# Kernel tuning notes

Measured on AMD Instinct MI355X. Metric: run time of the kernel, lower is better.

## Reference

```python
import jax, jax.numpy as jnp
import numpy as np

NUM_HEADS = 8

def setup_inputs() -> dict:
    key = jax.random.key(0)
    ks = jax.random.split(key, 12)
    B, C, H, W = 4, 256, 64, 64
    QK = 256
    NSP = 256
    x = jax.random.normal(ks[0], (B, C, H, W), dtype=jnp.float32)
    affinity_matrix = jax.random.uniform(ks[1], (B, NSP, H * W), dtype=jnp.float32)
    norm_w = 1.0 + 0.02 * jax.random.normal(ks[2], (C,), dtype=jnp.float32)
    norm_b = 0.02 * jax.random.normal(ks[3], (C,), dtype=jnp.float32)
    Wq = 0.02 * jax.random.normal(ks[4], (QK, C), dtype=jnp.float32)
    Wk = 0.02 * jax.random.normal(ks[5], (QK, C), dtype=jnp.float32)
    Wv = 0.02 * jax.random.normal(ks[6], (C, C), dtype=jnp.float32)
    Wsp = 0.02 * jax.random.normal(ks[7], (QK, C), dtype=jnp.float32)
    lepe_w = 0.02 * jax.random.normal(ks[8], (C, 1, 3, 3), dtype=jnp.float32)  # depthwise OIHW
    lepe_b = 0.02 * jax.random.normal(ks[9], (C,), dtype=jnp.float32)
    return {"x": x, "affinity_matrix": affinity_matrix, "norm_w": norm_w,
            "norm_b": norm_b, "Wq": Wq, "Wk": Wk, "Wv": Wv, "Wsp": Wsp,
            "lepe_w": lepe_w, "lepe_b": lepe_b, "num_spixels": NSP}


def _layernorm2d(x, w, b, eps=1e-6):
    # LayerNorm over channel dim of NCHW input
    xp = x.transpose(0, 2, 3, 1)  # B,H,W,C
    mu = xp.mean(-1, keepdims=True)
    var = ((xp - mu) ** 2).mean(-1, keepdims=True)
    xn = (xp - mu) * jax.lax.rsqrt(var + eps) * w + b
    return xn.transpose(0, 3, 1, 2)


def _sgca(x, affinity_matrix, norm_w, norm_b, Wq, Wk, Wv, Wsp, lepe_w, lepe_b, num_spixels):
    B, C, H, W = x.shape
    HW = H * W
    h = NUM_HEADS
    qk_dim = Wq.shape[0]
    dqk = qk_dim // h
    dv = C // h
    scale = (C // h) ** -0.5

    xn = _layernorm2d(x, norm_w, norm_b)

    # superpixel aggregation: b (hw) c
    x_flat = xn.reshape(B, C, HW).transpose(0, 2, 1)  # B,HW,C
    stoken = jnp.einsum('bmn,bnc->bmc', affinity_matrix, x_flat)
    stoken = stoken / (affinity_matrix.sum(-1, keepdims=True) + 1e-16)  # B,nsp,C

    # sp projection -> B,h,dqk,nsp
    st = jnp.einsum('bmc,qc->bmq', stoken, Wsp).transpose(0, 2, 1)
    st = st.reshape(B, h, dqk, num_spixels)

    # 1x1 conv projections
    q = jnp.einsum('oc,bchw->bohw', Wq, xn).reshape(B, h, dqk, HW)
    k = jnp.einsum('oc,bchw->bohw', Wk, xn).reshape(B, h, dqk, HW)
    vx = jnp.einsum('oc,bchw->bohw', Wv, xn)  # B,C,H,W
    v = vx.reshape(B, h, dv, HW)

    # LePE: depthwise 3x3 conv on v(x)
    lepe = jax.lax.conv_general_dilated(
        vx, lepe_w, window_strides=(1, 1), padding=((1, 1), (1, 1)),
        feature_group_count=C, dimension_numbers=('NCHW', 'OIHW', 'NCHW'))
    lepe = lepe + lepe_b[None, :, None, None]
    # faithful to original: [B,C,HW] -> permute -> [B,HW,C] -> reshape B,C,H,W
    lepe = lepe.reshape(B, C, HW).transpose(0, 2, 1).reshape(B, C, H, W)

    # stage 1: k^T @ stoken, softmax over HW axis
    s_attn = jnp.einsum('bhdn,bhdm->bhnm', k, st) * scale  # B,h,HW,nsp
    s_attn = jax.nn.softmax(s_attn, axis=-2)
    s_out = jnp.einsum('bhdn,bhnm->bhdm', v, s_attn)  # B,h,dv,nsp

    # stage 2: stoken^T @ q, softmax over nsp axis
    x_attn = jnp.einsum('bhdm,bhdn->bhmn', st, q) * scale  # B,h,nsp,HW
    x_attn = jax.nn.softmax(x_attn, axis=-2)
    x_out = jnp.einsum('bhdm,bhmn->bhdn', s_out, x_attn).reshape(B, C, H, W)

    return x_out + lepe


def reference(x, affinity_matrix, norm_w, norm_b, Wq, Wk, Wv, Wsp, lepe_w, lepe_b, num_spixels):
    return _sgca(x, affinity_matrix, norm_w, norm_b, Wq, Wk, Wv, Wsp, lepe_w, lepe_b, num_spixels)
```

## Files before the change

### kernel.cpp

```cpp
#include <hip/hip_runtime.h>
#include <hip/hip_bf16.h>

#define BATCH 4
#define CCH   256
#define HWHW  4096
#define NSP   256
#define NHEAD 8
#define SCALE 0.17677669529663689f
#define PLANE 1048576L

typedef short bf16x8 __attribute__((ext_vector_type(8)));
typedef short bf16x4 __attribute__((ext_vector_type(4)));
typedef float f32x4  __attribute__((ext_vector_type(4)));

__device__ __forceinline__ short f2bs(float f) {
    __hip_bfloat16 h = __float2bfloat16(f);
    return *(short*)&h;
}
__device__ __forceinline__ bf16x8 cvt8(float4 a, float4 b) {
    bf16x8 p;
    p[0] = f2bs(a.x); p[1] = f2bs(a.y); p[2] = f2bs(a.z); p[3] = f2bs(a.w);
    p[4] = f2bs(b.x); p[5] = f2bs(b.y); p[6] = f2bs(b.z); p[7] = f2bs(b.w);
    return p;
}
__device__ __forceinline__ void gll16(const __hip_bfloat16* g, __hip_bfloat16* l) {
    __builtin_amdgcn_global_load_lds(
        (const __attribute__((address_space(1))) unsigned int*)(const void*)g,
        (__attribute__((address_space(3))) unsigned int*)(void*)l,
        16, 0, 0);
}

__global__ __launch_bounds__(512)
void ln_fused_kernel(const float* __restrict__ x, const float* __restrict__ w,
                     const float* __restrict__ bb,
                     const float* __restrict__ Wq, const float* __restrict__ Wk,
                     const float* __restrict__ Wv, const float* __restrict__ Wsp,
                     __hip_bfloat16* __restrict__ xn_cn,
                     __hip_bfloat16* __restrict__ xn_nc,
                     __hip_bfloat16* __restrict__ wbf)
{
    __shared__ float ps[32][64], pss[32][64];
    __shared__ float mus[64], rstds[64];
    __shared__ float wls[256], bls[256];
    int blk = blockIdx.x;
    int t = threadIdx.x;
    if (blk >= 256) {
        int sel = blk - 256;
        const float* src = (sel == 0) ? Wq : (sel == 1) ? Wk : (sel == 2) ? Wv : Wsp;
        __hip_bfloat16* dst = wbf + sel * 65536;
        for (int i = t * 4; i < 65536; i += 2048) {
            float4 f = *(const float4*)(src + i);
            __hip_bfloat16 p[4];
            p[0] = __float2bfloat16(f.x); p[1] = __float2bfloat16(f.y);
            p[2] = __float2bfloat16(f.z); p[3] = __float2bfloat16(f.w);
            *(int2*)(dst + i) = *(int2*)p;
        }
        return;
    }
    int b = blk >> 6;
    int n0 = (blk & 63) * 64;
    int pg = t & 15;
    int cq = t >> 4;
    if (t < 256) { wls[t] = w[t]; bls[t] = bb[t]; }

    const float* xp = x + ((long)(b * CCH + cq * 8)) * HWHW + n0 + pg * 4;
    float4 v[8];
#pragma unroll
    for (int i = 0; i < 8; ++i) v[i] = *(const float4*)(xp + (long)i * HWHW);
    float4 s = {0.f,0.f,0.f,0.f}, ss = {0.f,0.f,0.f,0.f};
#pragma unroll
    for (int i = 0; i < 8; ++i) {
        s.x += v[i].x; s.y += v[i].y; s.z += v[i].z; s.w += v[i].w;
        ss.x += v[i].x * v[i].x; ss.y += v[i].y * v[i].y;
        ss.z += v[i].z * v[i].z; ss.w += v[i].w * v[i].w;
    }
    *(float4*)&ps[cq][pg * 4]  = s;
    *(float4*)&pss[cq][pg * 4] = ss;
    __syncthreads();
    if (t < 64) {
        float S = 0.f, SS = 0.f;
#pragma unroll
        for (int q = 0; q < 32; ++q) { S += ps[q][t]; SS += pss[q][t]; }
        float mu = S * (1.f / 256.f);
        float var = SS * (1.f / 256.f) - mu * mu;
        mus[t] = mu; rstds[t] = rsqrtf(var + 1e-6f);
    }
    __syncthreads();
    float4 mu4 = *(float4*)&mus[pg * 4];
    float4 rs4 = *(float4*)&rstds[pg * 4];

    bf16x8 pk[4];
#pragma unroll
    for (int i = 0; i < 8; ++i) {
        int c = cq * 8 + i;
        float wc = wls[c], bc = bls[c];
        short h0 = f2bs((v[i].x - mu4.x) * rs4.x * wc + bc);
        short h1 = f2bs((v[i].y - mu4.y) * rs4.y * wc + bc);
        short h2 = f2bs((v[i].z - mu4.z) * rs4.z * wc + bc);
        short h3 = f2bs((v[i].w - mu4.w) * rs4.w * wc + bc);
        pk[0][i] = h0; pk[1][i] = h1; pk[2][i] = h2; pk[3][i] = h3;
        bf16x4 q; q[0] = h0; q[1] = h1; q[2] = h2; q[3] = h3;
        *(bf16x4*)(xn_cn + ((long)(b * CCH + c)) * HWHW + n0 + pg * 4) = q;
    }
#pragma unroll
    for (int j = 0; j < 4; ++j)
        *(bf16x8*)(xn_nc + ((long)b * HWHW + n0 + pg * 4 + j) * CCH + cq * 8) = pk[j];
}

__device__ __forceinline__ void gemm_k256_oneshot(
    const __hip_bfloat16* __restrict__ A, const __hip_bfloat16* __restrict__ B,
    __hip_bfloat16* __restrict__ C, int bx, int by, int bz,
    int N, long aStrideZ, long bStrideZ, long cStrideZ,
    __hip_bfloat16* __restrict__ Asm)
{
    const int K = 256;
    const int t = threadIdx.x, lane = t & 63, w = t >> 6;
    const int l15 = lane & 15, quad = lane >> 4;
    const int Mt = by * 64, Nt = bx * 64;
    const __hip_bfloat16* aSrc = A + (long)bz * aStrideZ
        + (long)(Mt + w * 16 + l15) * K + quad * 8;
#pragma unroll
    for (int p = 0; p < 8; ++p)
        gll16(aSrc + p * 32, Asm + ((w * 8 + p) << 9));

    const int wm = (w & 1) * 2, wn = (w >> 1) * 2;
    const __hip_bfloat16* b0p = B + (long)bz * bStrideZ
        + (long)(Nt + wn * 16 + l15) * K + quad * 8;
    const __hip_bfloat16* b1p = b0p + 16 * K;
    f32x4 acc00 = {0.f,0.f,0.f,0.f}, acc01 = acc00, acc10 = acc00, acc11 = acc00;
    __syncthreads();
#pragma unroll
    for (int s = 0; s < 8; ++s) {
        bf16x8 a0 = *(const bf16x8*)&Asm[((wm * 8 + s) << 9) + lane * 8];
        bf16x8 a1 = *(const bf16x8*)&Asm[(((wm + 1) * 8 + s) << 9) + lane * 8];
        bf16x8 b0 = *(const bf16x8*)(b0p + s * 32);
        bf16x8 b1 = *(const bf16x8*)(b1p + s * 32);
        acc00 = __builtin_amdgcn_mfma_f32_16x16x32_bf16(a0, b0, acc00, 0, 0, 0);
        acc01 = __builtin_amdgcn_mfma_f32_16x16x32_bf16(a0, b1, acc01, 0, 0, 0);
        acc10 = __builtin_amdgcn_mfma_f32_16x16x32_bf16(a1, b0, acc10, 0, 0, 0);
        acc11 = __builtin_amdgcn_mfma_f32_16x16x32_bf16(a1, b1, acc11, 0, 0, 0);
    }
    f32x4 accs[2][2] = {{acc00, acc01}, {acc10, acc11}};
#pragma unroll
    for (int i = 0; i < 2; ++i)
#pragma unroll
        for (int j = 0; j < 2; ++j)
#pragma unroll
            for (int r = 0; r < 4; ++r) {
                int m = Mt + (wm + i) * 16 + quad * 4 + r;
                int n = Nt + (wn + j) * 16 + l15;
                C[(long)bz * cStrideZ + (long)m * N + n] =
                    __float2bfloat16(accs[i][j][r]);
            }
}

template <int OUTK, int ASTAGE, bool ROWSUM, int NTL>
__device__ __forceinline__ void gemm_body(
    const void* __restrict__ Av, const __hip_bfloat16* __restrict__ B,
    void* __restrict__ Cptr, int bx, int by, int bz,
    int N, int K, int kChunk, int kShift,
    long aStrideZ, long bStrideZ, long cStrideZ,
    float* __restrict__ rsPart,
    __hip_bfloat16* __restrict__ Asm, __hip_bfloat16* __restrict__ Bsm,
    float* __restrict__ rsl)
{
    int z = bz;
    int b = z >> kShift;
    int ch = z & ((1 << kShift) - 1);
    int t = threadIdx.x;
    int lane = t & 63, w = t >> 6;
    int l15 = lane & 15, quad = lane >> 4;
    int Mt = by * 64, Nt = bx * 64 * NTL;

    if (ASTAGE == 2 && t < 64) {
        float s = 0.f;
#pragma unroll
        for (int pl = 0; pl < 8; ++pl) s += rsPart[((b * 8 + pl) << 8) + Mt + t];
        rsl[t] = s;
    }

    long aOff = (long)b * aStrideZ + (long)ch * kChunk
        + (long)(Mt + w * 16 + l15) * K + quad * 8;
    const float* aSrcF = (const float*)Av + aOff;
    const __hip_bfloat16* bSrc = B + (long)b * bStrideZ + (long)ch * kChunk
        + (long)(Nt + w * 16 + l15) * K + quad * 8;

    f32x4 acc[NTL][2][2];
#pragma unroll
    for (int nt = 0; nt < NTL; ++nt)
#pragma unroll
        for (int i = 0; i < 2; ++i)
#pragma unroll
            for (int j = 0; j < 2; ++j) acc[nt][i][j] = f32x4{0.f,0.f,0.f,0.f};
    f32x4 rs0 = {0.f,0.f,0.f,0.f}, rs1 = rs0;
    bf16x8 onesf;
    { short o = (l15 == 0) ? (short)0x3F80 : (short)0;
      onesf = bf16x8{o, o, o, o, o, o, o, o}; }
    int wm = (w & 1) * 2, wn = (w >> 1) * 2;

    float4 pf0, pf1, pf2, pf3;
    if (ASTAGE == 1) {
        pf0 = *(const float4*)(aSrcF);      pf1 = *(const float4*)(aSrcF + 4);
        pf2 = *(const float4*)(aSrcF + 32); pf3 = *(const float4*)(aSrcF + 36);
    }

    const bf16x8* AsmU = (const bf16x8*)Asm;
    const bf16x8* BsmU = (const bf16x8*)Bsm;

    for (int k0 = 0; k0 < kChunk; k0 += 64) {
        if (ASTAGE == 1) {
            *(bf16x8*)&Asm[t * 8]        = cvt8(pf0, pf1);
            *(bf16x8*)&Asm[2048 + t * 8] = cvt8(pf2, pf3);
        } else {
#pragma unroll
            for (int kh = 0; kh < 2; ++kh) {
                float4 s0 = {0.f,0.f,0.f,0.f}, s1 = {0.f,0.f,0.f,0.f};
#pragma unroll
                for (int pl = 0; pl < 8; ++pl) {
                    const float* p = aSrcF + (long)pl * 65536 + k0 + kh * 32;
                    float4 u0 = *(const float4*)p, u1 = *(const float4*)(p + 4);
                    s0.x += u0.x; s0.y += u0.y; s0.z += u0.z; s0.w += u0.w;
                    s1.x += u1.x; s1.y += u1.y; s1.z += u1.z; s1.w += u1.w;
                }
                *(bf16x8*)&Asm[kh * 2048 + t * 8] = cvt8(s0, s1);
            }
        }
#pragma unroll
        for (int nt = 0; nt < NTL; ++nt) {
            gll16(bSrc + (long)nt * 64 * K + k0,      Bsm + nt * 4096 + w * 512);
            gll16(bSrc + (long)nt * 64 * K + k0 + 32, Bsm + nt * 4096 + 2048 + w * 512);
        }
        __syncthreads();
        if (ASTAGE == 1 && k0 + 64 < kChunk) {
            const float* nx = aSrcF + k0 + 64;
            pf0 = *(const float4*)nx;        pf1 = *(const float4*)(nx + 4);
            pf2 = *(const float4*)(nx + 32); pf3 = *(const float4*)(nx + 36);
        }
#pragma unroll
        for (int kh = 0; kh < 2; ++kh) {
            bf16x8 a0 = AsmU[kh * 256 + wm * 64 + lane];
            bf16x8 a1 = AsmU[kh * 256 + (wm + 1) * 64 + lane];
            if (ROWSUM) {
                rs0 = __builtin_amdgcn_mfma_f32_16x16x32_bf16(a0, onesf, rs0, 0, 0, 0);
                rs1 = __builtin_amdgcn_mfma_f32_16x16x32_bf16(a1, onesf, rs1, 0, 0, 0);
            }
#pragma unroll
            for (int nt = 0; nt < NTL; ++nt) {
                bf16x8 b0 = BsmU[nt * 512 + kh * 256 + wn * 64 + lane];
                bf16x8 b1 = BsmU[nt * 512 + kh * 256 + (wn + 1) * 64 + lane];
                acc[nt][0][0] = __builtin_amdgcn_mfma_f32_16x16x32_bf16(a0, b0, acc[nt][0][0], 0, 0, 0);
                acc[nt][0][1] = __builtin_amdgcn_mfma_f32_16x16x32_bf16(a0, b1, acc[nt][0][1], 0, 0, 0);
                acc[nt][1][0] = __builtin_amdgcn_mfma_f32_16x16x32_bf16(a1, b0, acc[nt][1][0], 0, 0, 0);
                acc[nt][1][1] = __builtin_amdgcn_mfma_f32_16x16x32_bf16(a1, b1, acc[nt][1][1], 0, 0, 0);
            }
        }
        __syncthreads();
    }
    if (ROWSUM && bx == 0 && (w >> 1) == 0 && l15 == 0) {
#pragma unroll
        for (int r = 0; r < 4; ++r) {
            rsPart[(long)z * 256 + Mt + wm * 16 + quad * 4 + r]       = rs0[r];
            rsPart[(long)z * 256 + Mt + (wm + 1) * 16 + quad * 4 + r] = rs1[r];
        }
    }
#pragma unroll
    for (int nt = 0; nt < NTL; ++nt)
#pragma unroll
        for (int i = 0; i < 2; ++i)
#pragma unroll
            for (int j = 0; j < 2; ++j)
#pragma unroll
                for (int r = 0; r < 4; ++r) {
                    int m = Mt + (wm + i) * 16 + quad * 4 + r;
                    int n = Nt + nt * 64 + (wn + j) * 16 + l15;
                    float val = acc[nt][i][j][r];
                    if (ASTAGE == 2) val /= (rsl[m - Mt] + 1e-16f);
                    long off = (long)z * cStrideZ + (long)m * N + n;
                    if (OUTK == 0) ((float*)Cptr)[off] = val;
                    else ((__hip_bfloat16*)Cptr)[off] = __float2bfloat16(val);
                }
}

__global__ __launch_bounds__(256, 4)
void mega1_kernel(const float* __restrict__ aff,
                  const __hip_bfloat16* __restrict__ xn_cn,
                  const __hip_bfloat16* __restrict__ xn_nc,
                  const __hip_bfloat16* __restrict__ wbf,
                  __hip_bfloat16* __restrict__ qk_nc,
                  __hip_bfloat16* __restrict__ v_cn,
                  float* __restrict__ stoken_part,
                  float* __restrict__ rs_part)
{
    __shared__ __align__(16) char smem[40960];
    __hip_bfloat16* Asm = (__hip_bfloat16*)smem;
    __hip_bfloat16* Bsm = (__hip_bfloat16*)(smem + 8192);
    __hip_bfloat16* Aos = (__hip_bfloat16*)smem;
    int blk = blockIdx.x;
    if (blk < 128) {
        int i = blk;
        gemm_body<0, 1, true, 4>(aff, xn_cn, stoken_part,
            0, i & 3, i >> 2, 256, 4096, 512, 3,
            PLANE, PLANE, 65536L, rs_part, Asm, Bsm, nullptr);
    } else if (blk < 2176) {
        int i = blk - 128;
        gemm_k256_oneshot(xn_nc, wbf, qk_nc,
            i & 7, (i >> 3) & 63, i >> 9, 512, PLANE, 0L, 2 * PLANE, Aos);
    } else {
        int i = blk - 2176;
        gemm_k256_oneshot(wbf + 2 * 65536, xn_nc, v_cn,
            i & 63, (i >> 6) & 3, i >> 8, 4096, 0L, PLANE, PLANE, Aos);
    }
}

__global__ __launch_bounds__(256)
void stmd_kernel(const float* __restrict__ part,
                 const __hip_bfloat16* __restrict__ wsp,
                 __hip_bfloat16* __restrict__ st_md,
                 float* __restrict__ rs_part)
{
    __shared__ __hip_bfloat16 Asm[4096];
    __shared__ __hip_bfloat16 Bsm[4096];
    __shared__ float rsl[64];
    int i = blockIdx.x;
    gemm_body<1, 2, false, 1>(part, wsp, st_md,
        i & 3, (i >> 2) & 3, i >> 4, 256, 256, 256, 0,
        524288L, 0L, 65536L, rs_part, Asm, Bsm, rsl);
}

__device__ __forceinline__
void stage1_dev(char* smem, int chunk, int bh,
                const __hip_bfloat16* __restrict__ qk_nc,
                const __hip_bfloat16* __restrict__ v_cn,
                const __hip_bfloat16* __restrict__ st_md,
                __hip_bfloat16* __restrict__ opart)
{
    __hip_bfloat16* Es  = (__hip_bfloat16*)smem;
    __hip_bfloat16* sts = (__hip_bfloat16*)(smem + 36864);
    const int b = bh >> 3, h = bh & 7;
    const int t = threadIdx.x, lane = t & 63, w = t >> 6;
    const int l15 = lane & 15, quad = lane >> 4;
    const int n0 = chunk * 256;

    {
        const int4* src = (const int4*)(st_md + ((long)(b * 256 + t)) * 256 + h * 32);
        int4* dst = (int4*)&sts[t * 40];
        dst[0] = src[0]; dst[1] = src[1]; dst[2] = src[2]; dst[3] = src[3];
    }
    const __hip_bfloat16* kfp = qk_nc + ((long)b * 4096 + n0 + 16 * w + l15) * 512 + 256 + h * 32 + quad * 8;
    const __hip_bfloat16* vp0 = v_cn + ((long)(b * 256 + h * 32 + l15)) * 4096 + n0 + quad * 8;
    const __hip_bfloat16* vp1 = vp0 + 16 * 4096;
    bf16x8 kfs[4], vv[4][4];
    kfs[0]   = *(const bf16x8*)(kfp);
    vv[0][0] = *(const bf16x8*)(vp0);
    vv[0][1] = *(const bf16x8*)(vp1);
    vv[0][2] = *(const bf16x8*)(vp0 + 32);
    vv[0][3] = *(const bf16x8*)(vp1 + 32);
    __syncthreads();
    bf16x8 afrag[16];
#pragma unroll
    for (int mt = 0; mt < 16; ++mt)
        afrag[mt] = *(const bf16x8*)&sts[(mt * 16 + l15) * 40 + quad * 8];
    bf16x8 onesf;
    { short o = (l15 == 0) ? (short)0x3F80 : (short)0;
      onesf = bf16x8{o, o, o, o, o, o, o, o}; }

    f32x4 occ[4][3];
#pragma unroll
    for (int i = 0; i < 4; ++i)
#pragma unroll
        for (int j = 0; j < 3; ++j) occ[i][j] = f32x4{0.f,0.f,0.f,0.f};

#pragma unroll
    for (int sub = 0; sub < 4; ++sub) {
#pragma unroll
        for (int mt = 0; mt < 16; ++mt) {
            f32x4 s = __builtin_amdgcn_mfma_f32_16x16x32_bf16(afrag[mt], kfs[sub], f32x4{0.f,0.f,0.f,0.f}, 0, 0, 0);
#pragma unroll
            for (int r = 0; r < 4; ++r)
                Es[(mt * 16 + quad * 4 + r) * 72 + 16 * w + l15] =
                    __float2bfloat16(__expf(s[r] * SCALE));
        }
        if (sub < 3) {
            kfs[sub + 1]   = *(const bf16x8*)(kfp + (long)(sub + 1) * 64 * 512);
            vv[sub + 1][0] = *(const bf16x8*)(vp0 + (sub + 1) * 64);
            vv[sub + 1][1] = *(const bf16x8*)(vp1 + (sub + 1) * 64);
            vv[sub + 1][2] = *(const bf16x8*)(vp0 + (sub + 1) * 64 + 32);
            vv[sub + 1][3] = *(const bf16x8*)(vp1 + (sub + 1) * 64 + 32);
        }
        __syncthreads();
#pragma unroll
        for (int ks = 0; ks < 2; ++ks) {
            bf16x8 bf0 = vv[sub][2 * ks + 0];
            bf16x8 bf1 = vv[sub][2 * ks + 1];
#pragma unroll
            for (int mi = 0; mi < 4; ++mi) {
                bf16x8 af = *(const bf16x8*)&Es[(64 * w + mi * 16 + l15) * 72 + ks * 32 + quad * 8];
                occ[mi][0] = __builtin_amdgcn_mfma_f32_16x16x32_bf16(af, bf0, occ[mi][0], 0, 0, 0);
                occ[mi][1] = __builtin_amdgcn_mfma_f32_16x16x32_bf16(af, bf1, occ[mi][1], 0, 0, 0);
                occ[mi][2] = __builtin_amdgcn_mfma_f32_16x16x32_bf16(af, onesf, occ[mi][2], 0, 0, 0);
            }
        }
        __syncthreads();
    }
    __hip_bfloat16* tb = Es;
#pragma unroll
    for (int mi = 0; mi < 4; ++mi)
#pragma unroll
        for (int jt = 0; jt < 3; ++jt) {
            if (jt == 2 && l15 != 0) continue;
            int col = jt * 16 + l15;
#pragma unroll
            for (int r = 0; r < 4; ++r) {
                int m = 64 * w + mi * 16 + quad * 4 + r;
                tb[col * 264 + m] = __float2bfloat16(occ[mi][jt][r]);
            }
        }
    __syncthreads();
    int* og = (int*)(opart) + (long)(chunk * 32 + bh) * 4224;
    const int* tbi = (const int*)tb;
#pragma unroll
    for (int i = 0; i < 17; ++i) {
        int idx = t + i * 256;
        if (idx < 4224) {
            int row = idx >> 7, off = idx & 127;
            og[idx] = tbi[row * 132 + off];
        }
    }
}

__device__ __forceinline__
void lepe_dev(char* smem, int bx, int cy, int b,
              const __hip_bfloat16* __restrict__ v_cn,
              const float* __restrict__ lw, const float* __restrict__ lb,
              __hip_bfloat16* __restrict__ lepe_cn)
{
    __hip_bfloat16* in_t    = (__hip_bfloat16*)smem;
    __hip_bfloat16* tile_bf = (__hip_bfloat16*)(smem + 24576);
    float* wls = (float*)(smem + 41472);
    float* bls = (float*)(smem + 42624);
    const int c0 = cy * 32;
    const int t = threadIdx.x;
    const int n0 = bx * 256, r0 = bx * 4;

    for (int i = t; i < 288; i += 256) wls[i] = lw[c0 * 9 + i];
    if (t < 32)  bls[t] = lb[c0 + t];
#pragma unroll
    for (int i = 0; i < 6; ++i) {
        int vi = t + i * 256;
        int ch = vi / 48;
        int off = (vi % 48) * 8;
        int g = (r0 - 1) * 64 + off;
        int4 val = {0, 0, 0, 0};
        if ((unsigned)g < 4096u)
            val = *(const int4*)(v_cn + (((long)(b * CCH + c0 + ch)) << 12) + g);
        *(int4*)&in_t[ch * 384 + off] = val;
    }
    __syncthreads();

    const int lane = t & 63, w = t >> 6;
#pragma unroll
    for (int i = 0; i < 8; ++i) {
        int ch = w * 8 + i;
        float cr[6], lf[6], rf[6];
#pragma unroll
        for (int rr = 0; rr < 6; ++rr) {
            cr[rr] = (float)in_t[ch * 384 + rr * 64 + lane];
            float lv = __shfl_up(cr[rr], 1);
            float rv = __shfl_down(cr[rr], 1);
            lf[rr] = (lane == 0) ? 0.f : lv;
            rf[rr] = (lane == 63) ? 0.f : rv;
        }
        float w0 = wls[ch*9+0], w1 = wls[ch*9+1], w2 = wls[ch*9+2];
        float w3 = wls[ch*9+3], w4 = wls[ch*9+4], w5 = wls[ch*9+5];
        float w6 = wls[ch*9+6], w7 = wls[ch*9+7], w8 = wls[ch*9+8];
        float bias = bls[ch];
#pragma unroll
        for (int r = 0; r < 4; ++r) {
            float acc = bias
                + lf[r]   * w0 + cr[r]   * w1 + rf[r]   * w2
                + lf[r+1] * w3 + cr[r+1] * w4 + rf[r+1] * w5
                + lf[r+2] * w6 + cr[r+2] * w7 + rf[r+2] * w8;
            tile_bf[(r * 64 + lane) * 33 + ch] = __float2bfloat16(acc);
        }
    }
    __syncthreads();
#pragma unroll
    for (int i = 0; i < 32; ++i) {
        int idx = t + i * 256;
        int nl = idx >> 5, cj = idx & 31;
        int sp = n0 + nl;
        lepe_cn[((long)(b * CCH + (sp >> 4)) << 12) + (nl & 15) * 256 + c0 + cj] =
            tile_bf[nl * 33 + cj];
    }
}

__global__ __launch_bounds__(256)
void mega2_kernel(const __hip_bfloat16* __restrict__ qk_nc,
                  const __hip_bfloat16* __restrict__ v_cn,
                  const __hip_bfloat16* __restrict__ st_md,
                  __hip_bfloat16* __restrict__ opart,
                  const float* __restrict__ lw, const float* __restrict__ lb,
                  __hip_bfloat16* __restrict__ lepe_cn)
{
    __shared__ __align__(16) char smem[57344];
    int blk = blockIdx.x;
    if (blk < 512) {
        stage1_dev(smem, blk & 15, blk >> 4, qk_nc, v_cn, st_md, opart);
    } else {
        int j = blk - 512;
        lepe_dev(smem, j & 15, (j >> 4) & 7, j >> 7, v_cn, lw, lb, lepe_cn);
    }
}

__global__ __launch_bounds__(256)
void merge1_kernel(const __hip_bfloat16* __restrict__ opart, __hip_bfloat16* __restrict__ sout)
{
    int t = blockIdx.x * 256 + threadIdx.x;
    int m = t & 255;
    int d = (t >> 8) & 31;
    int bh = t >> 13;
    float num = 0.f, den = 0.f;
    for (int ch = 0; ch < 16; ++ch) {
        long base = (long)((ch * 32 + bh) * 33) * 256 + m;
        num += (float)opart[base + (long)d * 256];
        den += (float)opart[base + 32 * 256];
    }
    sout[(long)bh * 8192 + d * 256 + m] = __float2bfloat16(num / den);
}

__global__ __launch_bounds__(256)
void stage2_mfma(const __hip_bfloat16* __restrict__ qk_nc,
                 const __hip_bfloat16* __restrict__ st_md,
                 const __hip_bfloat16* __restrict__ sout_bf,
                 const __hip_bfloat16* __restrict__ lepe_cn,
                 float* __restrict__ out)
{
    __shared__ __hip_bfloat16 Es2[64 * 264];
    __shared__ __hip_bfloat16 sos[32 * 264];
    __shared__ float o_t[32 * 68];
    const int chunk = blockIdx.x, bh = blockIdx.y;
    const int b = bh >> 3, h = bh & 7;
    const int t = threadIdx.x, lane = t & 63, w = t >> 6;
    const int l15 = lane & 15, quad = lane >> 4;
    const int n0 = chunk * 256;

    {
        int row = t >> 3, seg = t & 7;
        const int4* src = (const int4*)(sout_bf + (long)bh * 8192 + row * 256 + seg * 32);
        int4* dst = (int4*)&sos[row * 264 + seg * 32];
        dst[0] = src[0]; dst[1] = src[1]; dst[2] = src[2]; dst[3] = src[3];
    }
    bf16x8 stfrag[4];
#pragma unroll
    for (int mt = 0; mt < 4; ++mt)
        stfrag[mt] = *(const bf16x8*)(st_md
            + ((long)(b * 256 + 64 * w + mt * 16 + l15)) * 256 + h * 32 + quad * 8);
    const __hip_bfloat16* qfp = qk_nc + ((long)b * 4096 + n0 + l15) * 512 + h * 32 + quad * 8;
    bf16x8 qq[4][4];
#pragma unroll
    for (int nt = 0; nt < 4; ++nt)
        qq[0][nt] = *(const bf16x8*)(qfp + (long)(nt * 16) * 512);
    bf16x8 onesf;
    { short o = (l15 == 0) ? (short)0x3F80 : (short)0;
      onesf = bf16x8{o, o, o, o, o, o, o, o}; }
    __syncthreads();

#pragma unroll
    for (int sub = 0; sub < 4; ++sub) {
        const int nbase = n0 + sub * 64;
#pragma unroll
        for (int nt = 0; nt < 4; ++nt) {
            bf16x8 qf = qq[sub][nt];
#pragma unroll
            for (int mt = 0; mt < 4; ++mt) {
                f32x4 s = __builtin_amdgcn_mfma_f32_16x16x32_bf16(qf, stfrag[mt], f32x4{0.f,0.f,0.f,0.f}, 0, 0, 0);
#pragma unroll
                for (int r = 0; r < 4; ++r)
                    Es2[(nt * 16 + quad * 4 + r) * 264 + 64 * w + mt * 16 + l15] =
                        __float2bfloat16(__expf(s[r] * SCALE));
            }
        }
        if (sub < 3) {
#pragma unroll
            for (int nt = 0; nt < 4; ++nt)
                qq[sub + 1][nt] = *(const bf16x8*)(qfp + (long)((sub + 1) * 64 + nt * 16) * 512);
        }
        __syncthreads();
        f32x4 o0 = {0.f,0.f,0.f,0.f}, o1 = o0, o2 = o0;
#pragma unroll
        for (int ks = 0; ks < 8; ++ks) {
            bf16x8 af = *(const bf16x8*)&Es2[(16 * w + l15) * 264 + ks * 32 + quad * 8];
            bf16x8 b0 = *(const bf16x8*)&sos[(l15) * 264 + ks * 32 + quad * 8];
            bf16x8 b1 = *(const bf16x8*)&sos[(16 + l15) * 264 + ks * 32 + quad * 8];
            o0 = __builtin_amdgcn_mfma_f32_16x16x32_bf16(af, b0, o0, 0, 0, 0);
            o1 = __builtin_amdgcn_mfma_f32_16x16x32_bf16(af, b1, o1, 0, 0, 0);
            o2 = __builtin_amdgcn_mfma_f32_16x16x32_bf16(af, onesf, o2, 0, 0, 0);
        }
        __syncthreads();
#pragma unroll
        for (int r = 0; r < 4; ++r) {
            float den = __shfl(o2[r], lane & 48);
            float inv = 1.f / den;
            o_t[(l15) * 68 + 16 * w + quad * 4 + r]      = o0[r] * inv;
            o_t[(16 + l15) * 68 + 16 * w + quad * 4 + r] = o1[r] * inv;
        }
        __syncthreads();
        {
            int row = t >> 3, coff = (t & 7) * 8;
            long gb = ((long)(b * 256 + h * 32 + row)) * 4096 + nbase + coff;
            int4 lp4 = *(const int4*)(lepe_cn + gb);
            const __hip_bfloat16* lp = (const __hip_bfloat16*)&lp4;
            const float* sp = &o_t[row * 68 + coff];
            float4 r0, r1;
            r0.x = sp[0] + (float)lp[0]; r0.y = sp[1] + (float)lp[1];
            r0.z = sp[2] + (float)lp[2]; r0.w = sp[3] + (float)lp[3];
            r1.x = sp[4] + (float)lp[4]; r1.y = sp[5] + (float)lp[5];
            r1.z = sp[6] + (float)lp[6]; r1.w = sp[7] + (float)lp[7];
            *(float4*)(out + gb)     = r0;
            *(float4*)(out + gb + 4) = r1;
        }
        __syncthreads();
    }
}

extern "C" void kernel_launch(void* const* d_in, const int* in_sizes, int n_in,
                              void* d_out, int out_size, void* d_ws, size_t ws_size,
                              hipStream_t stream)
{
    const float* x    = (const float*)d_in[0];
    const float* aff  = (const float*)d_in[1];
    const float* nw   = (const float*)d_in[2];
    const float* nb   = (const float*)d_in[3];
    const float* Wq   = (const float*)d_in[4];
    const float* Wk   = (const float*)d_in[5];
    const float* Wv   = (const float*)d_in[6];
    const float* Wsp  = (const float*)d_in[7];
    const float* lw   = (const float*)d_in[8];
    const float* lb   = (const float*)d_in[9];
    float* out = (float*)d_out;

    float* ws = (float*)d_ws;
    const long P = PLANE;
    __hip_bfloat16* qk_nc  = (__hip_bfloat16*)(ws);
    __hip_bfloat16* v_cn   = (__hip_bfloat16*)(ws + 4 * P);
    __hip_bfloat16* xn_cn  = (__hip_bfloat16*)(ws + 6 * P);
    __hip_bfloat16* xn_nc  = (__hip_bfloat16*)(ws + 8 * P);
    __hip_bfloat16* lepe_cn= (__hip_bfloat16*)(ws + 10 * P);
    float* stoken_part = ws + 14 * P;
    __hip_bfloat16* opart = (__hip_bfloat16*)(ws + 16 * P);
    float* tail        = ws + 16 * P + 2162688;
    __hip_bfloat16* wbf       = (__hip_bfloat16*)tail;
    __hip_bfloat16* st_md     = (__hip_bfloat16*)(tail + 262144);
    __hip_bfloat16* sout_bf   = (__hip_bfloat16*)(tail + 393216);
    float* rs_part = tail + 525312;

    ln_fused_kernel<<<260, 512, 0, stream>>>(x, nw, nb, Wq, Wk, Wv, Wsp,
                                             xn_cn, xn_nc, wbf);
    mega1_kernel<<<3200, 256, 0, stream>>>(aff, xn_cn, xn_nc, wbf,
                                           qk_nc, v_cn, stoken_part, rs_part);
    stmd_kernel<<<64, 256, 0, stream>>>(stoken_part, wbf + 3 * 65536, st_md, rs_part);
    mega2_kernel<<<1024, 256, 0, stream>>>(qk_nc, v_cn, st_md, opart, lw, lb, lepe_cn);
    merge1_kernel<<<1024, 256, 0, stream>>>(opart, sout_bf);
    stage2_mfma<<<dim3(16, 32), 256, 0, stream>>>(qk_nc, st_md, sout_bf, lepe_cn, out);
}
```

Measured before the change: 211.4 us.

## Enlarge projection GEMM tiles to 128x128 with register double-buffered B loads

The fused projection GEMMs (q/k and v) inside mega1 move from 64x64 tiles to 128x128 tiles, so each wave computes a 4x4 grid of MFMA fragments and reuses each A fragment against four B fragments. B operands are prefetched one k-step ahead in registers, the grid drops from 3200 to 896 blocks, and block-to-tile mapping is reordered, including the stoken GEMM batch/tile order. The aim is fewer redundant global loads per FLOP and less per-block overhead. In exchange LDS grows to 64KB and occupancy is lowered to 2 blocks per SM, which cuts latency hiding and leaves fewer blocks to balance load.

```diff
diff --git a/kernel.cpp b/kernel.cpp
--- a/kernel.cpp
+++ b/kernel.cpp
@@ -107,7 +107,7 @@
         *(bf16x8*)(xn_nc + ((long)b * HWHW + n0 + pg * 4 + j) * CCH + cq * 8) = pk[j];
 }
 
-__device__ __forceinline__ void gemm_k256_oneshot(
+__device__ __forceinline__ void gemm_k256_128(
     const __hip_bfloat16* __restrict__ A, const __hip_bfloat16* __restrict__ B,
     __hip_bfloat16* __restrict__ C, int bx, int by, int bz,
     int N, long aStrideZ, long bStrideZ, long cStrideZ,
@@ -116,41 +116,69 @@
     const int K = 256;
     const int t = threadIdx.x, lane = t & 63, w = t >> 6;
     const int l15 = lane & 15, quad = lane >> 4;
-    const int Mt = by * 64, Nt = bx * 64;
-    const __hip_bfloat16* aSrc = A + (long)bz * aStrideZ
-        + (long)(Mt + w * 16 + l15) * K + quad * 8;
-#pragma unroll
-    for (int p = 0; p < 8; ++p)
-        gll16(aSrc + p * 32, Asm + ((w * 8 + p) << 9));
-
-    const int wm = (w & 1) * 2, wn = (w >> 1) * 2;
-    const __hip_bfloat16* b0p = B + (long)bz * bStrideZ
-        + (long)(Nt + wn * 16 + l15) * K + quad * 8;
-    const __hip_bfloat16* b1p = b0p + 16 * K;
-    f32x4 acc00 = {0.f,0.f,0.f,0.f}, acc01 = acc00, acc10 = acc00, acc11 = acc00;
-    __syncthreads();
-#pragma unroll
-    for (int s = 0; s < 8; ++s) {
-        bf16x8 a0 = *(const bf16x8*)&Asm[((wm * 8 + s) << 9) + lane * 8];
-        bf16x8 a1 = *(const bf16x8*)&Asm[(((wm + 1) * 8 + s) << 9) + lane * 8];
-        bf16x8 b0 = *(const bf16x8*)(b0p + s * 32);
-        bf16x8 b1 = *(const bf16x8*)(b1p + s * 32);
-        acc00 = __builtin_amdgcn_mfma_f32_16x16x32_bf16(a0, b0, acc00, 0, 0, 0);
-        acc01 = __builtin_amdgcn_mfma_f32_16x16x32_bf16(a0, b1, acc01, 0, 0, 0);
-        acc10 = __builtin_amdgcn_mfma_f32_16x16x32_bf16(a1, b0, acc10, 0, 0, 0);
-        acc11 = __builtin_amdgcn_mfma_f32_16x16x32_bf16(a1, b1, acc11, 0, 0, 0);
-    }
-    f32x4 accs[2][2] = {{acc00, acc01}, {acc10, acc11}};
-#pragma unroll
-    for (int i = 0; i < 2; ++i)
-#pragma unroll
-        for (int j = 0; j < 2; ++j)
+    const int Mt = by * 128, Nt = bx * 128;
+    {
+        const __hip_bfloat16* aBase = A + (long)bz * aStrideZ
+            + (long)(Mt + l15) * K + quad * 8;
+#pragma unroll
+        for (int p = 0; p < 16; ++p) {
+            const int rt = w * 2 + (p >> 3), s = p & 7;
+            gll16(aBase + (long)(rt * 16) * K + s * 32, Asm + (rt * 8 + s) * 512);
+        }
+    }
+    const int wm2 = w & 1, wn2 = w >> 1;
+    const __hip_bfloat16* bBase = B + (long)bz * bStrideZ
+        + (long)(Nt + wn2 * 64 + l15) * K + quad * 8;
+
+    f32x4 acc[4][4];
+#pragma unroll
+    for (int mi = 0; mi < 4; ++mi)
+#pragma unroll
+        for (int nj = 0; nj < 4; ++nj) acc[mi][nj] = f32x4{0.f,0.f,0.f,0.f};
+
+    bf16x8 bEv[4], bOd[4];
+#pragma unroll
+    for (int nj = 0; nj < 4; ++nj)
+        bEv[nj] = *(const bf16x8*)(bBase + (long)(nj * 16) * K);
+    __syncthreads();
+#pragma unroll
+    for (int sp = 0; sp < 4; ++sp) {
+        const int s0 = 2 * sp, s1 = 2 * sp + 1;
+#pragma unroll
+        for (int nj = 0; nj < 4; ++nj)
+            bOd[nj] = *(const bf16x8*)(bBase + (long)(nj * 16) * K + s1 * 32);
+#pragma unroll
+        for (int mi = 0; mi < 4; ++mi) {
+            bf16x8 a = *(const bf16x8*)&Asm[((wm2 * 4 + mi) * 8 + s0) * 512 + lane * 8];
+            acc[mi][0] = __builtin_amdgcn_mfma_f32_16x16x32_bf16(a, bEv[0], acc[mi][0], 0, 0, 0);
+            acc[mi][1] = __builtin_amdgcn_mfma_f32_16x16x32_bf16(a, bEv[1], acc[mi][1], 0, 0, 0);
+            acc[mi][2] = __builtin_amdgcn_mfma_f32_16x16x32_bf16(a, bEv[2], acc[mi][2], 0, 0, 0);
+            acc[mi][3] = __builtin_amdgcn_mfma_f32_16x16x32_bf16(a, bEv[3], acc[mi][3], 0, 0, 0);
+        }
+        if (sp < 3) {
+#pragma unroll
+            for (int nj = 0; nj < 4; ++nj)
+                bEv[nj] = *(const bf16x8*)(bBase + (long)(nj * 16) * K + (s0 + 2) * 32);
+        }
+#pragma unroll
+        for (int mi = 0; mi < 4; ++mi) {
+            bf16x8 a = *(const bf16x8*)&Asm[((wm2 * 4 + mi) * 8 + s1) * 512 + lane * 8];
+            acc[mi][0] = __builtin_amdgcn_mfma_f32_16x16x32_bf16(a, bOd[0], acc[mi][0], 0, 0, 0);
+            acc[mi][1] = __builtin_amdgcn_mfma_f32_16x16x32_bf16(a, bOd[1], acc[mi][1], 0, 0, 0);
+            acc[mi][2] = __builtin_amdgcn_mfma_f32_16x16x32_bf16(a, bOd[2], acc[mi][2], 0, 0, 0);
+            acc[mi][3] = __builtin_amdgcn_mfma_f32_16x16x32_bf16(a, bOd[3], acc[mi][3], 0, 0, 0);
+        }
+    }
+#pragma unroll
+    for (int mi = 0; mi < 4; ++mi)
+#pragma unroll
+        for (int nj = 0; nj < 4; ++nj)
 #pragma unroll
             for (int r = 0; r < 4; ++r) {
-                int m = Mt + (wm + i) * 16 + quad * 4 + r;
-                int n = Nt + (wn + j) * 16 + l15;
+                int m = Mt + wm2 * 64 + mi * 16 + quad * 4 + r;
+                int n = Nt + wn2 * 64 + nj * 16 + l15;
                 C[(long)bz * cStrideZ + (long)m * N + n] =
-                    __float2bfloat16(accs[i][j][r]);
+                    __float2bfloat16(acc[mi][nj][r]);
             }
 }
 
@@ -281,7 +309,7 @@
                 }
 }
 
-__global__ __launch_bounds__(256, 4)
+__global__ __launch_bounds__(256, 2)
 void mega1_kernel(const float* __restrict__ aff,
                   const __hip_bfloat16* __restrict__ xn_cn,
                   const __hip_bfloat16* __restrict__ xn_nc,
@@ -291,24 +319,26 @@
                   float* __restrict__ stoken_part,
                   float* __restrict__ rs_part)
 {
-    __shared__ __align__(16) char smem[40960];
+    __shared__ __align__(16) char smem[65536];
     __hip_bfloat16* Asm = (__hip_bfloat16*)smem;
     __hip_bfloat16* Bsm = (__hip_bfloat16*)(smem + 8192);
-    __hip_bfloat16* Aos = (__hip_bfloat16*)smem;
+    __hip_bfloat16* A128 = (__hip_bfloat16*)smem;
     int blk = blockIdx.x;
     if (blk < 128) {
         int i = blk;
         gemm_body<0, 1, true, 4>(aff, xn_cn, stoken_part,
-            0, i & 3, i >> 2, 256, 4096, 512, 3,
+            0, i >> 5, i & 31, 256, 4096, 512, 3,
             PLANE, PLANE, 65536L, rs_part, Asm, Bsm, nullptr);
-    } else if (blk < 2176) {
+    } else if (blk < 640) {
         int i = blk - 128;
-        gemm_k256_oneshot(xn_nc, wbf, qk_nc,
-            i & 7, (i >> 3) & 63, i >> 9, 512, PLANE, 0L, 2 * PLANE, Aos);
+        int bx = i >> 7, rem = i & 127;
+        gemm_k256_128(xn_nc, wbf, qk_nc,
+            bx, rem >> 2, rem & 3, 512, PLANE, 0L, 2 * PLANE, A128);
     } else {
-        int i = blk - 2176;
-        gemm_k256_oneshot(wbf + 2 * 65536, xn_nc, v_cn,
-            i & 63, (i >> 6) & 3, i >> 8, 4096, 0L, PLANE, PLANE, Aos);
+        int i = blk - 640;
+        int by = i >> 7, rem = i & 127;
+        gemm_k256_128(wbf + 2 * 65536, xn_nc, v_cn,
+            rem >> 2, by, rem & 3, 4096, 0L, PLANE, PLANE, A128);
     }
 }
 
@@ -656,8 +686,8 @@
 
     ln_fused_kernel<<<260, 512, 0, stream>>>(x, nw, nb, Wq, Wk, Wv, Wsp,
                                              xn_cn, xn_nc, wbf);
-    mega1_kernel<<<3200, 256, 0, stream>>>(aff, xn_cn, xn_nc, wbf,
-                                           qk_nc, v_cn, stoken_part, rs_part);
+    mega1_kernel<<<896, 256, 0, stream>>>(aff, xn_cn, xn_nc, wbf,
+                                          qk_nc, v_cn, stoken_part, rs_part);
     stmd_kernel<<<64, 256, 0, stream>>>(stoken_part, wbf + 3 * 65536, st_md, rs_part);
     mega2_kernel<<<1024, 256, 0, stream>>>(qk_nc, v_cn, st_md, opart, lw, lb, lepe_cn);
     merge1_kernel<<<1024, 256, 0, stream>>>(opart, sout_bf);
```

Result: faster. 195.8 us (-7.4%).
